# Kernel optimization log

Hardware: AMD Instinct MI355X
Metric: run time of the kernel (lower is better)

Reference implementation:

```python
import jax, jax.numpy as jnp
import numpy as np

N_NODES = 50000
N_EDGES = 800000
N_SCALES = 4
D_IN = 128
D_HID = 128


def gcn_conv(x, W, b, src, dst, ew, n):
    # PyG GCNConv: h = x @ W; add self loops (weight 1); symmetric normalization
    # deg computed over destination with edge weights; out = scatter(norm * h[src]) + b
    h = x @ W
    loops = jnp.arange(n)
    src_f = jnp.concatenate([src, loops])
    dst_f = jnp.concatenate([dst, loops])
    ew_f = jnp.concatenate([ew, jnp.ones((n,), x.dtype)])
    deg = jax.ops.segment_sum(ew_f, dst_f, num_segments=n)
    dinv = jnp.where(deg > 0, jax.lax.rsqrt(deg), jnp.zeros((), x.dtype))
    norm = dinv[src_f] * ew_f * dinv[dst_f]  # [E+n]
    out = jax.ops.segment_sum(h[src_f] * norm[:, None], dst_f, num_segments=n)
    return out + b


def setup_inputs() -> dict:
    key = jax.random.key(0)
    ks = jax.random.split(key, 8)
    x = jax.random.normal(ks[0], (N_NODES, D_IN), dtype=jnp.float32)
    edge_index = jax.random.randint(ks[1], (N_SCALES, 2, N_EDGES), 0, N_NODES, dtype=jnp.int64)
    edge_weight = jax.random.uniform(ks[2], (N_SCALES, N_EDGES), dtype=jnp.float32)
    s = 1.0 / np.sqrt(D_IN)
    W0 = jax.random.uniform(ks[3], (D_IN, D_HID), jnp.float32, -s, s)
    b0 = jnp.zeros((D_HID,), jnp.float32)
    W1 = jax.random.uniform(ks[4], (D_HID, D_HID), jnp.float32, -s, s)
    b1 = jnp.zeros((D_HID,), jnp.float32)
    prelu_a = 0.25 * jnp.ones((D_HID,), jnp.float32)  # torch PReLU default init
    return {"x": x, "edge_index": edge_index, "edge_weight": edge_weight,
            "W0": W0, "b0": b0, "W1": W1, "b1": b1, "prelu_a": prelu_a}


def reference(x, edge_index, edge_weight, W0, b0, W1, b1, prelu_a):
    n = x.shape[0]
    prelu = lambda z: jnp.where(z > 0, z, prelu_a * z)
    outs = []
    for t in range(edge_index.shape[0]):  # small fixed number of scales
        src, dst = edge_index[t, 0], edge_index[t, 1]
        ew = edge_weight[t]
        z = prelu(gcn_conv(x, W0, b0, src, dst, ew, n))
        z = prelu(gcn_conv(z, W1, b1, src, dst, ew, n))
        outs.append(z)
    return jnp.stack(outs)  # [nm_scale, N, hidden]
```

## Files before the change

### kernel.cpp

```cpp
#include <hip/hip_runtime.h>

#define NN 50000
#define NE 800000
#define NS 4
#define NT (NS * NN)
#define D 128
#define SB2 782
#define EW_SCALE 262144.0f
#define EW_INV (1.0f / 262144.0f)

typedef unsigned long long ull;
typedef __attribute__((ext_vector_type(8))) short bf16x8;
typedef __attribute__((ext_vector_type(4))) float f32x4;

__device__ __forceinline__ unsigned short f2bf(float f) {
  unsigned int u = __float_as_uint(f);
  u += 0x7fffu + ((u >> 16) & 1u);
  return (unsigned short)(u >> 16);
}
__device__ __forceinline__ float bf2f(unsigned short h) {
  return __uint_as_float((unsigned int)h << 16);
}


__global__ __launch_bounds__(256) void gemm_plain_bf16out(
    const float* __restrict__ X, const float* __restrict__ W,
    unsigned short* __restrict__ O, int M) {
  __shared__ float xs[64 * 130];
  __shared__ float ws[32 * 128];
  const int tid = threadIdx.x;
  const int r0 = blockIdx.x * 64;
  for (int i = tid; i < 64 * 64; i += 256) {
    int row = i >> 6, kh = i & 63;
    float2 v = make_float2(0.f, 0.f);
    int gr = r0 + row;
    if (gr < M) v = *(const float2*)&X[(size_t)gr * D + kh * 2];
    *(float2*)&xs[row * 130 + kh * 2] = v;
  }
  const int tx = tid & 15, ty = tid >> 4;
  const int c0 = tx * 4;
  const int c1 = 64 + tx * 4;
  float acc[4][8];
#pragma unroll
  for (int i = 0; i < 4; i++)
#pragma unroll
    for (int j = 0; j < 8; j++) acc[i][j] = 0.f;

  for (int kc = 0; kc < 4; kc++) {
    __syncthreads();
    for (int i = tid; i < 32 * 32; i += 256) {
      ((float4*)ws)[i] = ((const float4*)(W + kc * 32 * D))[i];
    }
    __syncthreads();
#pragma unroll 4
    for (int k2 = 0; k2 < 32; k2++) {
      const int k = kc * 32 + k2;
      float a[4];
#pragma unroll
      for (int j = 0; j < 4; j++) a[j] = xs[(ty * 4 + j) * 130 + k];
      float4 b0 = *(const float4*)&ws[k2 * 128 + c0];
      float4 b1 = *(const float4*)&ws[k2 * 128 + c1];
      float b[8] = {b0.x, b0.y, b0.z, b0.w, b1.x, b1.y, b1.z, b1.w};
#pragma unroll
      for (int i = 0; i < 4; i++)
#pragma unroll
        for (int j = 0; j < 8; j++) acc[i][j] += a[i] * b[j];
    }
  }
#pragma unroll
  for (int i = 0; i < 4; i++) {
    int gr = r0 + ty * 4 + i;
    if (gr < M) {
      ushort4 o0, o1;
      o0.x = f2bf(acc[i][0]); o0.y = f2bf(acc[i][1]);
      o0.z = f2bf(acc[i][2]); o0.w = f2bf(acc[i][3]);
      o1.x = f2bf(acc[i][4]); o1.y = f2bf(acc[i][5]);
      o1.z = f2bf(acc[i][6]); o1.w = f2bf(acc[i][7]);
      *(ushort4*)&O[(size_t)gr * D + c0] = o0;
      *(ushort4*)&O[(size_t)gr * D + c1] = o1;
    }
  }
}

__global__ __launch_bounds__(256) void prep_w1_k(const float* __restrict__ W,
                                                 unsigned short* __restrict__ Wsw) {
  int idx = blockIdx.x * 256 + threadIdx.x;
  int j = idx & 7, lane = (idx >> 3) & 63, s = (idx >> 9) & 3, bn = idx >> 11;
  float v = W[(s * 32 + ((lane >> 4) * 8) + j) * D + bn * 16 + (lane & 15)];
  unsigned short hi = f2bf(v);
  float lo = v - bf2f(hi);
  Wsw[idx] = hi;
  Wsw[16384 + idx] = f2bf(lo);
}

__global__ __launch_bounds__(256) void gemm_inplace_mfma_k(
    unsigned short* __restrict__ ZhA, const unsigned short* __restrict__ Wsw) {
  const int t = blockIdx.y;
  unsigned short* Z = ZhA + (size_t)t * NN * D;
  const int tid = threadIdx.x;
  const int wv = tid >> 6, l = tid & 63;
  const int r0 = blockIdx.x * 64 + wv * 16;
  const int mrow = r0 + (l & 15);
  const int arow = mrow < NN ? mrow : NN - 1;
  bf16x8 a[4];
#pragma unroll
  for (int s = 0; s < 4; s++)
    a[s] = *(const bf16x8*)&Z[(size_t)arow * D + s * 32 + (l >> 4) * 8];
  const int orow0 = r0 + (l >> 4) * 4;
#pragma unroll
  for (int bn = 0; bn < 8; bn++) {
    f32x4 acc = {0.f, 0.f, 0.f, 0.f};
#pragma unroll
    for (int s = 0; s < 4; s++) {
      bf16x8 blo = *(const bf16x8*)&Wsw[16384 + ((bn * 4 + s) * 64 + l) * 8];
      bf16x8 bhi = *(const bf16x8*)&Wsw[((bn * 4 + s) * 64 + l) * 8];
      acc = __builtin_amdgcn_mfma_f32_16x16x32_bf16(a[s], blo, acc, 0, 0, 0);
      acc = __builtin_amdgcn_mfma_f32_16x16x32_bf16(a[s], bhi, acc, 0, 0, 0);
    }
    const int col = bn * 16 + (l & 15);
#pragma unroll
    for (int i = 0; i < 4; i++) {
      int row = orow0 + i;
      if (row < NN) Z[(size_t)row * D + col] = f2bf(acc[i]);
    }
  }
}


__global__ __launch_bounds__(256) void initp_k(ull* __restrict__ packed, int n) {
  int i = blockIdx.x * 256 + threadIdx.x;
  if (i < n) packed[i] = 0ULL;
}

__global__ __launch_bounds__(256) void countpos_all_k(const int* __restrict__ ei,
                                                      const float* __restrict__ ewA,
                                                      ull* __restrict__ packedA,
                                                      int* __restrict__ posA) {
  const int t = blockIdx.y;
  const int e0 = blockIdx.x * 1024 + threadIdx.x;
  const int* dst = ei + (size_t)t * 2 * NE + NE;
  const float* ew = ewA + (size_t)t * NE;
  int d[4];
  float w[4];
  bool va[4];
#pragma unroll
  for (int q = 0; q < 4; q++) {
    int e = e0 + q * 256;
    va[q] = e < NE;
    d[q] = 0;
    w[q] = 0.f;
    if (va[q]) {
      d[q] = dst[e];
      w[q] = ew[e];
    }
  }
  ull old[4];
#pragma unroll
  for (int q = 0; q < 4; q++) {
    if (va[q]) {
      ull add = (1ULL << 32) | (ull)__float2uint_rn(w[q] * EW_SCALE);
      old[q] = atomicAdd(&packedA[t * NN + d[q]], add);
    }
  }
#pragma unroll
  for (int q = 0; q < 4; q++) {
    if (va[q]) posA[(size_t)t * NE + e0 + q * 256] = (int)(old[q] >> 32);
  }
}

__global__ __launch_bounds__(256) void unpack_scan_k(const ull* __restrict__ packedA,
                                                     float* __restrict__ dinvA,
                                                     int* __restrict__ cntA,
                                                     int* __restrict__ partial) {
  __shared__ int sm[256];
  const int tid = threadIdx.x;
  const int i = blockIdx.x * 256 + tid;
  int c = 0;
  if (i < NT) {
    ull p = packedA[i];
    c = (int)(p >> 32);
    cntA[i] = c;
    float deg = 1.0f + (float)(unsigned int)(p & 0xffffffffULL) * EW_INV;
    dinvA[i] = rsqrtf(deg);
  }
  sm[tid] = c;
  __syncthreads();
  for (int off = 128; off > 0; off >>= 1) {
    if (tid < off) sm[tid] += sm[tid + off];
    __syncthreads();
  }
  if (tid == 0) partial[blockIdx.x] = sm[0];
}

__global__ __launch_bounds__(256) void scan_top_k(const int* __restrict__ partial,
                                                  int* __restrict__ poffs, int nb) {
  __shared__ int sm[256];
  const int t = threadIdx.x;
  const int chunk = (nb + 255) >> 8;
  const int lo = t * chunk;
  const int hi = min(lo + chunk, nb);
  int s = 0;
  for (int i = lo; i < hi; i++) s += partial[i];
  sm[t] = s;
  __syncthreads();
  for (int off = 1; off < 256; off <<= 1) {
    int u = (t >= off) ? sm[t - off] : 0;
    __syncthreads();
    sm[t] += u;
    __syncthreads();
  }
  int run = sm[t] - s;
  for (int i = lo; i < hi; i++) {
    poffs[i] = run;
    run += partial[i];
  }
}

__global__ __launch_bounds__(256) void scan_write_k(const int* __restrict__ cntA,
                                                    const int* __restrict__ poffs,
                                                    int* __restrict__ offsA) {
  __shared__ int sm[256];
  const int t = threadIdx.x;
  const int i = blockIdx.x * 256 + t;
  int v = (i < NT) ? cntA[i] : 0;
  sm[t] = v;
  __syncthreads();
  for (int off = 1; off < 256; off <<= 1) {
    int u = (t >= off) ? sm[t - off] : 0;
    __syncthreads();
    sm[t] += u;
    __syncthreads();
  }
  if (i < NT) offsA[i] = poffs[blockIdx.x] + sm[t] - v;
}

__global__ __launch_bounds__(256) void fill_all_k(const int* __restrict__ ei,
                                                  const float* __restrict__ ewA,
                                                  const float* __restrict__ dinvA,
                                                  const int* __restrict__ offsA,
                                                  const int* __restrict__ posA,
                                                  int2* __restrict__ eeA) {
  const int t = blockIdx.y;
  const int e = blockIdx.x * 256 + threadIdx.x;
  if (e < NE) {
    const int* src = ei + (size_t)t * 2 * NE;
    const int* dst = src + NE;
    int s = src[e], d = dst[e];
    float w = ewA[(size_t)t * NE + e] * dinvA[t * NN + s] * dinvA[t * NN + d];
    eeA[offsA[t * NN + d] + posA[(size_t)t * NE + e]] = make_int2(s, __float_as_int(w));
  }
}

__global__ __launch_bounds__(256) void gather1_all_k(
    const unsigned short* __restrict__ H, const int* __restrict__ offsA,
    const int* __restrict__ cntA, const int2* __restrict__ eeA,
    const float* __restrict__ dinvA, const float* __restrict__ bias,
    const float* __restrict__ pa, unsigned short* __restrict__ ZhA) {
  const int t = blockIdx.y;
  int g = blockIdx.x * 256 + threadIdx.x;
  int wid = g >> 5;
  int lane = g & 31;
  if (wid >= NN) return;
  const int base = t * NN + wid;
  const int st = offsA[base];
  const int len = cntA[base];
  const int c = lane * 4;
  float ax = 0.f, ay = 0.f, az = 0.f, aw = 0.f;
  int j = 0;
  for (; j + 8 <= len; j += 8) {
    int2 p0 = eeA[st + j];
    int2 p1 = eeA[st + j + 1];
    int2 p2 = eeA[st + j + 2];
    int2 p3 = eeA[st + j + 3];
    int2 p4 = eeA[st + j + 4];
    int2 p5 = eeA[st + j + 5];
    int2 p6 = eeA[st + j + 6];
    int2 p7 = eeA[st + j + 7];
    ushort4 v0 = *(const ushort4*)&H[(size_t)p0.x * D + c];
    ushort4 v1 = *(const ushort4*)&H[(size_t)p1.x * D + c];
    ushort4 v2 = *(const ushort4*)&H[(size_t)p2.x * D + c];
    ushort4 v3 = *(const ushort4*)&H[(size_t)p3.x * D + c];
    ushort4 v4 = *(const ushort4*)&H[(size_t)p4.x * D + c];
    ushort4 v5 = *(const ushort4*)&H[(size_t)p5.x * D + c];
    ushort4 v6 = *(const ushort4*)&H[(size_t)p6.x * D + c];
    ushort4 v7 = *(const ushort4*)&H[(size_t)p7.x * D + c];
    float w0 = __int_as_float(p0.y), w1 = __int_as_float(p1.y);
    float w2 = __int_as_float(p2.y), w3 = __int_as_float(p3.y);
    float w4 = __int_as_float(p4.y), w5 = __int_as_float(p5.y);
    float w6 = __int_as_float(p6.y), w7 = __int_as_float(p7.y);
    ax += w0 * bf2f(v0.x) + w1 * bf2f(v1.x) + w2 * bf2f(v2.x) + w3 * bf2f(v3.x);
    ay += w0 * bf2f(v0.y) + w1 * bf2f(v1.y) + w2 * bf2f(v2.y) + w3 * bf2f(v3.y);
    az += w0 * bf2f(v0.z) + w1 * bf2f(v1.z) + w2 * bf2f(v2.z) + w3 * bf2f(v3.z);
    aw += w0 * bf2f(v0.w) + w1 * bf2f(v1.w) + w2 * bf2f(v2.w) + w3 * bf2f(v3.w);
    ax += w4 * bf2f(v4.x) + w5 * bf2f(v5.x) + w6 * bf2f(v6.x) + w7 * bf2f(v7.x);
    ay += w4 * bf2f(v4.y) + w5 * bf2f(v5.y) + w6 * bf2f(v6.y) + w7 * bf2f(v7.y);
    az += w4 * bf2f(v4.z) + w5 * bf2f(v5.z) + w6 * bf2f(v6.z) + w7 * bf2f(v7.z);
    aw += w4 * bf2f(v4.w) + w5 * bf2f(v5.w) + w6 * bf2f(v6.w) + w7 * bf2f(v7.w);
  }
  for (; j + 4 <= len; j += 4) {
    int2 p0 = eeA[st + j];
    int2 p1 = eeA[st + j + 1];
    int2 p2 = eeA[st + j + 2];
    int2 p3 = eeA[st + j + 3];
    ushort4 v0 = *(const ushort4*)&H[(size_t)p0.x * D + c];
    ushort4 v1 = *(const ushort4*)&H[(size_t)p1.x * D + c];
    ushort4 v2 = *(const ushort4*)&H[(size_t)p2.x * D + c];
    ushort4 v3 = *(const ushort4*)&H[(size_t)p3.x * D + c];
    float w0 = __int_as_float(p0.y), w1 = __int_as_float(p1.y);
    float w2 = __int_as_float(p2.y), w3 = __int_as_float(p3.y);
    ax += w0 * bf2f(v0.x) + w1 * bf2f(v1.x) + w2 * bf2f(v2.x) + w3 * bf2f(v3.x);
    ay += w0 * bf2f(v0.y) + w1 * bf2f(v1.y) + w2 * bf2f(v2.y) + w3 * bf2f(v3.y);
    az += w0 * bf2f(v0.z) + w1 * bf2f(v1.z) + w2 * bf2f(v2.z) + w3 * bf2f(v3.z);
    aw += w0 * bf2f(v0.w) + w1 * bf2f(v1.w) + w2 * bf2f(v2.w) + w3 * bf2f(v3.w);
  }
  for (; j < len; j++) {
    int2 p = eeA[st + j];
    float w = __int_as_float(p.y);
    ushort4 v = *(const ushort4*)&H[(size_t)p.x * D + c];
    ax += w * bf2f(v.x);
    ay += w * bf2f(v.y);
    az += w * bf2f(v.z);
    aw += w * bf2f(v.w);
  }
  float dv = dinvA[base];
  float d2 = dv * dv;
  ushort4 h = *(const ushort4*)&H[(size_t)wid * D + c];
  ax += d2 * bf2f(h.x) + bias[c];
  ay += d2 * bf2f(h.y) + bias[c + 1];
  az += d2 * bf2f(h.z) + bias[c + 2];
  aw += d2 * bf2f(h.w) + bias[c + 3];
  ax = ax > 0.f ? ax : pa[c] * ax;
  ay = ay > 0.f ? ay : pa[c + 1] * ay;
  az = az > 0.f ? az : pa[c + 2] * az;
  aw = aw > 0.f ? aw : pa[c + 3] * aw;
  ushort4 o;
  o.x = f2bf(ax); o.y = f2bf(ay); o.z = f2bf(az); o.w = f2bf(aw);
  *(ushort4*)&ZhA[(size_t)t * NN * D + (size_t)wid * D + c] = o;
}

__global__ __launch_bounds__(256) void gather2_all_k(
    const unsigned short* __restrict__ YA, const int* __restrict__ offsA,
    const int* __restrict__ cntA, const int2* __restrict__ eeA,
    const float* __restrict__ dinvA, const float* __restrict__ bias,
    const float* __restrict__ pa, float* __restrict__ out) {
  const int t = blockIdx.y;
  int g = blockIdx.x * 256 + threadIdx.x;
  int wid = g >> 5;
  int lane = g & 31;
  if (wid >= NN) return;
  const unsigned short* Y = YA + (size_t)t * NN * D;
  const int base = t * NN + wid;
  const int st = offsA[base];
  const int len = cntA[base];
  const int c = lane * 4;
  float ax = 0.f, ay = 0.f, az = 0.f, aw = 0.f;
  int j = 0;
  for (; j + 8 <= len; j += 8) {
    int2 p0 = eeA[st + j];
    int2 p1 = eeA[st + j + 1];
    int2 p2 = eeA[st + j + 2];
    int2 p3 = eeA[st + j + 3];
    int2 p4 = eeA[st + j + 4];
    int2 p5 = eeA[st + j + 5];
    int2 p6 = eeA[st + j + 6];
    int2 p7 = eeA[st + j + 7];
    ushort4 v0 = *(const ushort4*)&Y[(size_t)p0.x * D + c];
    ushort4 v1 = *(const ushort4*)&Y[(size_t)p1.x * D + c];
    ushort4 v2 = *(const ushort4*)&Y[(size_t)p2.x * D + c];
    ushort4 v3 = *(const ushort4*)&Y[(size_t)p3.x * D + c];
    ushort4 v4 = *(const ushort4*)&Y[(size_t)p4.x * D + c];
    ushort4 v5 = *(const ushort4*)&Y[(size_t)p5.x * D + c];
    ushort4 v6 = *(const ushort4*)&Y[(size_t)p6.x * D + c];
    ushort4 v7 = *(const ushort4*)&Y[(size_t)p7.x * D + c];
    float w0 = __int_as_float(p0.y), w1 = __int_as_float(p1.y);
    float w2 = __int_as_float(p2.y), w3 = __int_as_float(p3.y);
    float w4 = __int_as_float(p4.y), w5 = __int_as_float(p5.y);
    float w6 = __int_as_float(p6.y), w7 = __int_as_float(p7.y);
    ax += w0 * bf2f(v0.x) + w1 * bf2f(v1.x) + w2 * bf2f(v2.x) + w3 * bf2f(v3.x);
    ay += w0 * bf2f(v0.y) + w1 * bf2f(v1.y) + w2 * bf2f(v2.y) + w3 * bf2f(v3.y);
    az += w0 * bf2f(v0.z) + w1 * bf2f(v1.z) + w2 * bf2f(v2.z) + w3 * bf2f(v3.z);
    aw += w0 * bf2f(v0.w) + w1 * bf2f(v1.w) + w2 * bf2f(v2.w) + w3 * bf2f(v3.w);
    ax += w4 * bf2f(v4.x) + w5 * bf2f(v5.x) + w6 * bf2f(v6.x) + w7 * bf2f(v7.x);
    ay += w4 * bf2f(v4.y) + w5 * bf2f(v5.y) + w6 * bf2f(v6.y) + w7 * bf2f(v7.y);
    az += w4 * bf2f(v4.z) + w5 * bf2f(v5.z) + w6 * bf2f(v6.z) + w7 * bf2f(v7.z);
    aw += w4 * bf2f(v4.w) + w5 * bf2f(v5.w) + w6 * bf2f(v6.w) + w7 * bf2f(v7.w);
  }
  for (; j + 4 <= len; j += 4) {
    int2 p0 = eeA[st + j];
    int2 p1 = eeA[st + j + 1];
    int2 p2 = eeA[st + j + 2];
    int2 p3 = eeA[st + j + 3];
    ushort4 v0 = *(const ushort4*)&Y[(size_t)p0.x * D + c];
    ushort4 v1 = *(const ushort4*)&Y[(size_t)p1.x * D + c];
    ushort4 v2 = *(const ushort4*)&Y[(size_t)p2.x * D + c];
    ushort4 v3 = *(const ushort4*)&Y[(size_t)p3.x * D + c];
    float w0 = __int_as_float(p0.y), w1 = __int_as_float(p1.y);
    float w2 = __int_as_float(p2.y), w3 = __int_as_float(p3.y);
    ax += w0 * bf2f(v0.x) + w1 * bf2f(v1.x) + w2 * bf2f(v2.x) + w3 * bf2f(v3.x);
    ay += w0 * bf2f(v0.y) + w1 * bf2f(v1.y) + w2 * bf2f(v2.y) + w3 * bf2f(v3.y);
    az += w0 * bf2f(v0.z) + w1 * bf2f(v1.z) + w2 * bf2f(v2.z) + w3 * bf2f(v3.z);
    aw += w0 * bf2f(v0.w) + w1 * bf2f(v1.w) + w2 * bf2f(v2.w) + w3 * bf2f(v3.w);
  }
  for (; j < len; j++) {
    int2 p = eeA[st + j];
    float w = __int_as_float(p.y);
    ushort4 v = *(const ushort4*)&Y[(size_t)p.x * D + c];
    ax += w * bf2f(v.x);
    ay += w * bf2f(v.y);
    az += w * bf2f(v.z);
    aw += w * bf2f(v.w);
  }
  float dv = dinvA[base];
  float d2 = dv * dv;
  ushort4 h = *(const ushort4*)&Y[(size_t)wid * D + c];
  ax += d2 * bf2f(h.x) + bias[c];
  ay += d2 * bf2f(h.y) + bias[c + 1];
  az += d2 * bf2f(h.z) + bias[c + 2];
  aw += d2 * bf2f(h.w) + bias[c + 3];
  ax = ax > 0.f ? ax : pa[c] * ax;
  ay = ay > 0.f ? ay : pa[c + 1] * ay;
  az = az > 0.f ? az : pa[c + 2] * az;
  aw = aw > 0.f ? aw : pa[c + 3] * aw;
  float* outT = out + (size_t)t * NN * D;
  *(float4*)&outT[(size_t)wid * D + c] = make_float4(ax, ay, az, aw);
}


extern "C" void kernel_launch(void* const* d_in, const int* in_sizes, int n_in,
                              void* d_out, int out_size, void* d_ws, size_t ws_size,
                              hipStream_t stream) {
  const float* x = (const float*)d_in[0];
  const int* ei = (const int*)d_in[1];
  const float* ew = (const float*)d_in[2];
  const float* W0 = (const float*)d_in[3];
  const float* b0 = (const float*)d_in[4];
  const float* W1 = (const float*)d_in[5];
  const float* b1 = (const float*)d_in[6];
  const float* pa = (const float*)d_in[7];
  float* out = (float*)d_out;

  ull* packedA = (ull*)d_ws;
  int2* eeA = (int2*)(packedA + NT);
  int* posA = (int*)(eeA + (size_t)NS * NE);
  float* dinvA = (float*)(posA + (size_t)NS * NE);
  int* cntA = (int*)(dinvA + NT);
  int* offsA = cntA + NT;
  int* partial = offsA + NT;
  int* poffs = partial + 1024;
  unsigned short* H0h = (unsigned short*)(poffs + 1024);
  unsigned short* ZhA = H0h + (size_t)NN * D;
  unsigned short* Wsw = ZhA + (size_t)NS * NN * D;

  const int gGemm = (NN + 63) / 64;
  const int gEdge = (NE + 255) / 256;
  const int gEdge4 = (NE + 1023) / 1024;
  const int gInit = (NT + 255) / 256;
  const int gGather = (NN * 32 + 255) / 256;

  gemm_plain_bf16out<<<gGemm, 256, 0, stream>>>(x, W0, H0h, NN);
  prep_w1_k<<<64, 256, 0, stream>>>(W1, Wsw);

  initp_k<<<gInit, 256, 0, stream>>>(packedA, NT);
  countpos_all_k<<<dim3(gEdge4, NS), 256, 0, stream>>>(ei, ew, packedA, posA);
  unpack_scan_k<<<SB2, 256, 0, stream>>>(packedA, dinvA, cntA, partial);
  scan_top_k<<<1, 256, 0, stream>>>(partial, poffs, SB2);
  scan_write_k<<<SB2, 256, 0, stream>>>(cntA, poffs, offsA);
  fill_all_k<<<dim3(gEdge, NS), 256, 0, stream>>>(ei, ew, dinvA, offsA, posA, eeA);

  gather1_all_k<<<dim3(gGather, NS), 256, 0, stream>>>(H0h, offsA, cntA, eeA,
                                                       dinvA, b0, pa, ZhA);
  gemm_inplace_mfma_k<<<dim3(gGemm, NS), 256, 0, stream>>>(ZhA, Wsw);
  gather2_all_k<<<dim3(gGather, NS), 256, 0, stream>>>(ZhA, offsA, cntA, eeA,
                                                       dinvA, b1, pa, out);
}
```

Before: 713.7 us.

## Split degree-count atomics across eight counter copies to reduce contention

Edge-degree atomic accumulation now goes to one of eight replicated counter arrays, chosen by block index. This spreads the 64-bit atomics over more addresses and cuts same-address contention. The unpack kernel sums the eight copies and records per-copy base offsets as 16-bit values, which the fill kernel adds to compute each edge's CSR slot. The counter buffers reuse the later GEMM/gather scratch regions, so the CSR build is moved ahead of the first GEMM. The cost is an 8x larger zero-init and more reads in the unpack kernel.

Measured after the change: 728.6 us. +2.1%, slower.

```diff
diff --git a/kernel.cpp b/kernel.cpp
--- a/kernel.cpp
+++ b/kernel.cpp
@@ -134,10 +134,11 @@
 
 __global__ __launch_bounds__(256) void countpos_all_k(const int* __restrict__ ei,
                                                       const float* __restrict__ ewA,
-                                                      ull* __restrict__ packedA,
+                                                      ull* __restrict__ pack8,
                                                       int* __restrict__ posA) {
   const int t = blockIdx.y;
   const int e0 = blockIdx.x * 1024 + threadIdx.x;
+  const size_t cOff = (size_t)(blockIdx.x & 7) * NT;
   const int* dst = ei + (size_t)t * 2 * NE + NE;
   const float* ew = ewA + (size_t)t * NE;
   int d[4];
@@ -159,7 +160,7 @@
   for (int q = 0; q < 4; q++) {
     if (va[q]) {
       ull add = (1ULL << 32) | (ull)__float2uint_rn(w[q] * EW_SCALE);
-      old[q] = atomicAdd(&packedA[t * NN + d[q]], add);
+      old[q] = atomicAdd(&pack8[cOff + t * NN + d[q]], add);
     }
   }
 #pragma unroll
@@ -168,19 +169,28 @@
   }
 }
 
-__global__ __launch_bounds__(256) void unpack_scan_k(const ull* __restrict__ packedA,
+__global__ __launch_bounds__(256) void unpack_scan_k(const ull* __restrict__ pack8,
                                                      float* __restrict__ dinvA,
                                                      int* __restrict__ cntA,
+                                                     unsigned short* __restrict__ cbase8,
                                                      int* __restrict__ partial) {
   __shared__ int sm[256];
   const int tid = threadIdx.x;
   const int i = blockIdx.x * 256 + tid;
   int c = 0;
   if (i < NT) {
-    ull p = packedA[i];
-    c = (int)(p >> 32);
+    unsigned int wsum = 0;
+    int run = 0;
+#pragma unroll
+    for (int k = 0; k < 8; k++) {
+      ull p = pack8[(size_t)k * NT + i];
+      cbase8[(size_t)k * NT + i] = (unsigned short)run;
+      run += (int)(p >> 32);
+      wsum += (unsigned int)(p & 0xffffffffULL);
+    }
+    c = run;
     cntA[i] = c;
-    float deg = 1.0f + (float)(unsigned int)(p & 0xffffffffULL) * EW_INV;
+    float deg = 1.0f + (float)wsum * EW_INV;
     dinvA[i] = rsqrtf(deg);
   }
   sm[tid] = c;
@@ -239,6 +249,7 @@
                                                   const float* __restrict__ dinvA,
                                                   const int* __restrict__ offsA,
                                                   const int* __restrict__ posA,
+                                                  const unsigned short* __restrict__ cbase8,
                                                   int2* __restrict__ eeA) {
   const int t = blockIdx.y;
   const int e = blockIdx.x * 256 + threadIdx.x;
@@ -246,8 +257,11 @@
     const int* src = ei + (size_t)t * 2 * NE;
     const int* dst = src + NE;
     int s = src[e], d = dst[e];
-    float w = ewA[(size_t)t * NE + e] * dinvA[t * NN + s] * dinvA[t * NN + d];
-    eeA[offsA[t * NN + d] + posA[(size_t)t * NE + e]] = make_int2(s, __float_as_int(w));
+    const int base = t * NN + d;
+    const size_t cOff = (size_t)((e >> 10) & 7) * NT;
+    float w = ewA[(size_t)t * NE + e] * dinvA[t * NN + s] * dinvA[base];
+    int slot = offsA[base] + (int)cbase8[cOff + base] + posA[(size_t)t * NE + e];
+    eeA[slot] = make_int2(s, __float_as_int(w));
   }
 }
 
@@ -439,8 +453,7 @@
   const float* pa = (const float*)d_in[7];
   float* out = (float*)d_out;
 
-  ull* packedA = (ull*)d_ws;
-  int2* eeA = (int2*)(packedA + NT);
+  int2* eeA = (int2*)d_ws;
   int* posA = (int*)(eeA + (size_t)NS * NE);
   float* dinvA = (float*)(posA + (size_t)NS * NE);
   int* cntA = (int*)(dinvA + NT);
@@ -450,22 +463,25 @@
   unsigned short* H0h = (unsigned short*)(poffs + 1024);
   unsigned short* ZhA = H0h + (size_t)NN * D;
   unsigned short* Wsw = ZhA + (size_t)NS * NN * D;
+  ull* pack8 = (ull*)H0h;
+  unsigned short* cbase8 = ZhA;
 
   const int gGemm = (NN + 63) / 64;
   const int gEdge = (NE + 255) / 256;
   const int gEdge4 = (NE + 1023) / 1024;
-  const int gInit = (NT + 255) / 256;
+  const int gInit8 = (8 * NT) / 256;
   const int gGather = (NN * 32 + 255) / 256;
+
+  initp_k<<<gInit8, 256, 0, stream>>>(pack8, 8 * NT);
+  countpos_all_k<<<dim3(gEdge4, NS), 256, 0, stream>>>(ei, ew, pack8, posA);
+  unpack_scan_k<<<SB2, 256, 0, stream>>>(pack8, dinvA, cntA, cbase8, partial);
+  scan_top_k<<<1, 256, 0, stream>>>(partial, poffs, SB2);
+  scan_write_k<<<SB2, 256, 0, stream>>>(cntA, poffs, offsA);
+  fill_all_k<<<dim3(gEdge, NS), 256, 0, stream>>>(ei, ew, dinvA, offsA, posA,
+                                                  cbase8, eeA);
 
   gemm_plain_bf16out<<<gGemm, 256, 0, stream>>>(x, W0, H0h, NN);
   prep_w1_k<<<64, 256, 0, stream>>>(W1, Wsw);
-
-  initp_k<<<gInit, 256, 0, stream>>>(packedA, NT);
-  countpos_all_k<<<dim3(gEdge4, NS), 256, 0, stream>>>(ei, ew, packedA, posA);
-  unpack_scan_k<<<SB2, 256, 0, stream>>>(packedA, dinvA, cntA, partial);
-  scan_top_k<<<1, 256, 0, stream>>>(partial, poffs, SB2);
-  scan_write_k<<<SB2, 256, 0, stream>>>(cntA, poffs, offsA);
-  fill_all_k<<<dim3(gEdge, NS), 256, 0, stream>>>(ei, ew, dinvA, offsA, posA, eeA);
 
   gather1_all_k<<<dim3(gGather, NS), 256, 0, stream>>>(H0h, offsA, cntA, eeA,
                                                        dinvA, b0, pa, ZhA);
```
